# Kernel optimization log

Hardware: AMD Instinct MI355X
Metric: run time of the kernel (lower is better)

The kernel has to match this reference:

```python
import jax, jax.numpy as jnp
import numpy as np

N_SRC, N_DST, N_EDGES = 50000, 50000, 500000
IN_DIM, OUT_DIM, EDGE_DIM = 128, 128, 11
BN_EPS = 1e-5


def setup_inputs() -> dict:
    key = jax.random.key(0)
    ks = jax.random.split(key, 16)
    s = 0.05
    return {
        "src_feat": jax.random.normal(ks[0], (N_SRC, IN_DIM), jnp.float32),
        "dst_feat": jax.random.normal(ks[1], (N_DST, IN_DIM), jnp.float32),
        "edge_feats": jax.random.normal(ks[2], (N_EDGES, EDGE_DIM), jnp.float32),
        "src_idx": jax.random.randint(ks[3], (N_EDGES,), 0, N_SRC, jnp.int32),
        "dst_idx": jax.random.randint(ks[4], (N_EDGES,), 0, N_DST, jnp.int32),
        "W_src": jax.random.normal(ks[5], (IN_DIM, OUT_DIM), jnp.float32) * s,
        "b_src": jnp.zeros((OUT_DIM,), jnp.float32),
        "W_dst": jax.random.normal(ks[6], (IN_DIM, OUT_DIM), jnp.float32) * s,
        "b_dst": jnp.zeros((OUT_DIM,), jnp.float32),
        "W_edge": jax.random.normal(ks[7], (EDGE_DIM, OUT_DIM), jnp.float32) * s,
        "b_edge": jnp.zeros((OUT_DIM,), jnp.float32),
        "attn_w": jax.random.normal(ks[8], (3 * OUT_DIM,), jnp.float32) * s,
        "attn_b": jnp.zeros((), jnp.float32),
        "gamma": jnp.ones((OUT_DIM,), jnp.float32),
        "beta": jnp.zeros((OUT_DIM,), jnp.float32),
        "alpha": jnp.asarray(0.25, jnp.float32),
    }


def reference(src_feat, dst_feat, edge_feats, src_idx, dst_idx,
              W_src, b_src, W_dst, b_dst, W_edge, b_edge,
              attn_w, attn_b, gamma, beta, alpha):
    D = W_src.shape[1]
    # project at node/edge level (math identical to projecting gathered feats)
    hs = src_feat @ W_src + b_src            # [Ns, D]  (linear_src)
    hd = dst_feat @ W_dst + b_dst            # [Nd, D]  (linear_dst)
    ep = edge_feats @ W_edge + b_edge        # [E, D]   (linear_edge)
    # attn_l on concat([src, dst, edge]) == sum of three dot products + bias
    aw_s, aw_d, aw_e = attn_w[:D], attn_w[D:2 * D], attn_w[2 * D:]
    a = (hs @ aw_s)[src_idx] + (hd @ aw_d)[dst_idx] + ep @ aw_e + attn_b  # [E]
    # edge softmax over incoming edges of each dst node
    n_dst = dst_feat.shape[0]
    seg_max = jax.ops.segment_max(a, dst_idx, num_segments=n_dst)
    a_exp = jnp.exp(a - seg_max[dst_idx])
    denom = jax.ops.segment_sum(a_exp, dst_idx, num_segments=n_dst)
    attn = a_exp / denom[dst_idx]            # [E]
    # weighted message = attn * linear_src(src_h); scatter-sum to dst
    msg = attn[:, None] * hs[src_idx]        # [E, D]
    h_new = jax.ops.segment_sum(msg, dst_idx, num_segments=n_dst)  # [Nd, D]
    # BatchNorm1d (training-mode batch statistics)
    mean = jnp.mean(h_new, axis=0)
    var = jnp.var(h_new, axis=0)
    h_bn = (h_new - mean) / jnp.sqrt(var + BN_EPS) * gamma + beta
    # PReLU (single shared alpha); dropout is identity in eval
    return jnp.where(h_bn >= 0, h_bn, alpha * h_bn)
```

## Files before the change

kernel.cpp:

```cpp
#include <hip/hip_runtime.h>
#include <cstddef>

#define NSRC 50000
#define NDST 50000
#define NEDGE 500000
#define DIM 128
#define EDIM 11
#define BN_EPS 1e-5f
#define SCAN_NBLK ((NDST + 255) / 256)

#define HS_BLOCKS ((NSRC + 63) / 64)
#define SCORE_BLK ((NDST + 63) / 64)
#define EDB       ((NEDGE + 511) / 512)
#define SC_BLOCKS ((NEDGE + 1023) / 1024)
#define FUSE_GRID (196 * 9)

typedef short bf16x8 __attribute__((ext_vector_type(8)));
typedef float f32x4 __attribute__((ext_vector_type(4)));

#define OFF_HS       0
#define OFF_SSCORE   (OFF_HS + (size_t)NSRC*DIM/2)
#define OFF_DSCORE   (OFF_SSCORE + NSRC)
#define OFF_DEG16    (OFF_DSCORE + NDST)
#define OFF_COLSUM   (OFF_DEG16 + (size_t)NDST*16)
#define OFF_COLSQ    (OFF_COLSUM + 128)
#define OFF_OFFS     (OFF_COLSQ + 128)
#define OFF_REW      (OFF_OFFS + NDST + 2)
#define OFF_PAIRS    (OFF_REW + 2*(size_t)NEDGE)
#define OFF_WDVEC    (OFF_PAIRS + 2*(size_t)NEDGE)
#define OFF_WEVEC    (OFF_WDVEC + 128)
#define OFF_SCAL     (OFF_WEVEC + 16)
#define OFF_WSVEC    (OFF_SCAL + 4)
#define OFF_PART     (OFF_WSVEC + 128)
#define OFF_WT       (((OFF_PART + 256 + 3) / 4) * 4)

__device__ __forceinline__ unsigned short f2bf(float x) {
    unsigned int u = __float_as_uint(x);
    u += 0x7FFFu + ((u >> 16) & 1u);
    return (unsigned short)(u >> 16);
}
__device__ __forceinline__ float bf2f(unsigned int u16) {
    return __uint_as_float(u16 << 16);
}

__global__ __launch_bounds__(256) void k_prepwt(const float* __restrict__ W_dst,
                                                const float* __restrict__ b_dst,
                                                const float* __restrict__ W_edge,
                                                const float* __restrict__ b_edge,
                                                const float* __restrict__ W_src,
                                                const float* __restrict__ b_src,
                                                const float* __restrict__ attn_w,
                                                const float* __restrict__ attn_b,
                                                float* __restrict__ wd_vec,
                                                float* __restrict__ we_vec,
                                                float* __restrict__ ws_vec,
                                                float* __restrict__ scal,
                                                unsigned short* __restrict__ wt) {
    int bb = blockIdx.x;
    int t = threadIdx.x;
    __shared__ float red[128];
    __shared__ float tile[32][33];
    if (bb == 0) {
        if (t < 128) {
            float acc = 0.f;
            for (int d = 0; d < DIM; ++d) acc += W_dst[t * DIM + d] * attn_w[DIM + d];
            wd_vec[t] = acc;
            red[t] = b_dst[t] * attn_w[DIM + t];
        }
        __syncthreads();
        for (int s = 64; s > 0; s >>= 1) { if (t < s) red[t] += red[t + s]; __syncthreads(); }
        if (t == 0) scal[0] = red[0];
    } else if (bb == 1) {
        if (t < 128) {
            if (t < EDIM) {
                float e = 0.f;
                for (int d = 0; d < DIM; ++d) e += W_edge[t * DIM + d] * attn_w[2 * DIM + d];
                we_vec[t] = e;
            }
            red[t] = b_edge[t] * attn_w[2 * DIM + t];
        }
        __syncthreads();
        for (int s = 64; s > 0; s >>= 1) { if (t < s) red[t] += red[t + s]; __syncthreads(); }
        if (t == 0) scal[1] = red[0] + attn_b[0];
    } else if (bb == 2) {
        if (t < 128) {
            float acc = 0.f;
            for (int d = 0; d < DIM; ++d) acc += W_src[t * DIM + d] * attn_w[d];
            ws_vec[t] = acc;
            red[t] = b_src[t] * attn_w[t];
        }
        __syncthreads();
        for (int s = 64; s > 0; s >>= 1) { if (t < s) red[t] += red[t + s]; __syncthreads(); }
        if (t == 0) scal[2] = red[0];
    } else {
        int idx = bb - 3;
        int bi = idx & 3;
        int bj = idx >> 2;
        int cl = t & 31;
        #pragma unroll
        for (int i = 0; i < 4; ++i) {
            int kl = (t >> 5) * 4 + i;
            tile[kl][cl] = W_src[(size_t)(bi * 32 + kl) * DIM + bj * 32 + cl];
        }
        __syncthreads();
        int ko = t & 31;
        #pragma unroll
        for (int i = 0; i < 4; ++i) {
            int co = (t >> 5) * 4 + i;
            wt[(size_t)(bj * 32 + co) * DIM + bi * 32 + ko] = f2bf(tile[ko][co]);
        }
    }
}

__global__ __launch_bounds__(256) void k_score(const float* __restrict__ src_feat,
                                               const float* __restrict__ dst_feat,
                                               const float* __restrict__ ws_vec,
                                               const float* __restrict__ wd_vec,
                                               const float* __restrict__ scal,
                                               float* __restrict__ s_score,
                                               float* __restrict__ d_score) {
    int bid = blockIdx.x;
    const float* X;
    const float* V;
    float* out;
    float c;
    int r0;
    if (bid < SCORE_BLK) {
        X = src_feat; V = ws_vec; out = s_score; c = scal[2]; r0 = bid * 64;
    } else {
        X = dst_feat; V = wd_vec; out = d_score; c = scal[0]; r0 = (bid - SCORE_BLK) * 64;
    }
    int t = threadIdx.x;
    int row = r0 + (t >> 2);
    int c0 = (t & 3) * 32;
    if (row >= NDST) return;
    const float4* x = reinterpret_cast<const float4*>(X + (size_t)row * DIM + c0);
    const float4* w = reinterpret_cast<const float4*>(V + c0);
    float p = 0.f;
    #pragma unroll
    for (int i = 0; i < 8; ++i) {
        float4 a = x[i], b = w[i];
        p += a.x * b.x + a.y * b.y + a.z * b.z + a.w * b.w;
    }
    p += __shfl_xor(p, 1);
    p += __shfl_xor(p, 2);
    if ((t & 3) == 0) out[row] = p + c;
}

__global__ __launch_bounds__(256, 2) void k_fused(const float* __restrict__ A,
                                               const unsigned short* __restrict__ wt,
                                               const float* __restrict__ bias,
                                               const float* __restrict__ ef,
                                               const int* __restrict__ src_idx,
                                               const int* __restrict__ dst_idx,
                                               const float* __restrict__ s_score,
                                               const float* __restrict__ d_score,
                                               const float* __restrict__ we_vec,
                                               const float* __restrict__ scal,
                                               unsigned short* __restrict__ hsb,
                                               int2* __restrict__ rew,
                                               int* __restrict__ deg16) {
    const int g = blockIdx.x / 9;
    const int sl = blockIdx.x % 9;
    const int t = threadIdx.x;

    if (sl < 4) {
        const int hb = g * 4 + sl;
        if (hb >= HS_BLOCKS) return;
        const int wv = t >> 6;
        const int lane = t & 63;
        const int lrow = lane & 15;
        const int kg = lane >> 4;
        const int grow = hb * 64 + wv * 16 + lrow;
        const bool rowok = grow < NSRC;
        const float* arow = A + (size_t)grow * DIM;

        bf16x8 af[4];
        #pragma unroll
        for (int s = 0; s < 4; ++s) {
            float4 p0 = make_float4(0.f, 0.f, 0.f, 0.f), p1 = p0;
            if (rowok) {
                p0 = *reinterpret_cast<const float4*>(arow + 32 * s + kg * 8);
                p1 = *reinterpret_cast<const float4*>(arow + 32 * s + kg * 8 + 4);
            }
            bf16x8 a;
            a[0] = (short)f2bf(p0.x); a[1] = (short)f2bf(p0.y);
            a[2] = (short)f2bf(p0.z); a[3] = (short)f2bf(p0.w);
            a[4] = (short)f2bf(p1.x); a[5] = (short)f2bf(p1.y);
            a[6] = (short)f2bf(p1.z); a[7] = (short)f2bf(p1.w);
            af[s] = a;
        }

        f32x4 acc[8];
        #pragma unroll
        for (int c = 0; c < 8; ++c) acc[c] = (f32x4){0.f, 0.f, 0.f, 0.f};

        #pragma unroll
        for (int c = 0; c < 8; ++c) {
            #pragma unroll
            for (int s = 0; s < 4; ++s) {
                const bf16x8 b = *reinterpret_cast<const bf16x8*>(
                    wt + ((size_t)(16 * c + lrow) * DIM + 32 * s + kg * 8));
                acc[c] = __builtin_amdgcn_mfma_f32_16x16x32_bf16(af[s], b, acc[c], 0, 0, 0);
            }
        }

        const int orow0 = hb * 64 + wv * 16 + kg * 4;
        #pragma unroll
        for (int c = 0; c < 8; ++c) {
            float bb = bias[16 * c + lrow];
            #pragma unroll
            for (int i = 0; i < 4; ++i) {
                unsigned int mybf = f2bf(acc[c][i] + bb);
                unsigned int nb = (unsigned int)__shfl_xor((int)mybf, 1);
                int orow = orow0 + i;
                if ((lrow & 1) == 0 && orow < NSRC) {
                    *reinterpret_cast<unsigned int*>(hsb + (size_t)orow * DIM + 16 * c + lrow)
                        = (mybf & 0xFFFFu) | (nb << 16);
                }
            }
        }
    } else {
        const int eb = g * 5 + (sl - 4);
        if (eb >= EDB) return;
        float wvv[EDIM];
        #pragma unroll
        for (int k = 0; k < EDIM; ++k) wvv[k] = we_vec[k];
        const float s1 = scal[1];
        int ebase = eb * 512 + t;
        #pragma unroll
        for (int i = 0; i < 2; ++i) {
            int e = ebase + i * 256;
            if (e < NEDGE) {
                int s = src_idx[e], d = dst_idx[e];
                const float* er = ef + (size_t)e * EDIM;
                float a = s1;
                #pragma unroll
                for (int k = 0; k < EDIM; ++k) a += er[k] * wvv[k];
                a += s_score[s] + d_score[d];
                float w = expf(a);
                int r = atomicAdd(&deg16[(size_t)d * 16], 1);
                rew[e] = make_int2(r, __float_as_int(w));
            }
        }
    }
}

__global__ __launch_bounds__(256) void k_scanA(const int* __restrict__ deg16,
                                               int* __restrict__ offL,
                                               int* __restrict__ partials) {
    __shared__ int tmp[256];
    int t = threadIdx.x;
    int i = blockIdx.x * 256 + t;
    int v = (i < NDST) ? deg16[(size_t)i * 16] : 0;
    tmp[t] = v;
    __syncthreads();
    #pragma unroll
    for (int d = 1; d < 256; d <<= 1) {
        int u = (t >= d) ? tmp[t - d] : 0;
        __syncthreads();
        tmp[t] += u;
        __syncthreads();
    }
    if (i < NDST) offL[i] = tmp[t] - v;
    if (t == 255) partials[blockIdx.x] = tmp[255];
}

__global__ __launch_bounds__(256) void k_scanB(int* __restrict__ partials) {
    __shared__ int tmp[256];
    int t = threadIdx.x;
    int v = (t < SCAN_NBLK) ? partials[t] : 0;
    tmp[t] = v;
    __syncthreads();
    #pragma unroll
    for (int d = 1; d < 256; d <<= 1) {
        int u = (t >= d) ? tmp[t - d] : 0;
        __syncthreads();
        tmp[t] += u;
        __syncthreads();
    }
    if (t < SCAN_NBLK) partials[t] = tmp[t] - v;
}

__global__ __launch_bounds__(256) void k_scat(const int* __restrict__ src_idx,
                                              const int* __restrict__ dst_idx,
                                              const int2* __restrict__ rew,
                                              const int* __restrict__ offL,
                                              const int* __restrict__ part,
                                              int2* __restrict__ pairs) {
    int base = blockIdx.x * 1024 + threadIdx.x;
    #pragma unroll
    for (int i = 0; i < 4; ++i) {
        int e = base + i * 256;
        if (e < NEDGE) {
            int d = dst_idx[e];
            int2 r = rew[e];
            int pos = offL[d] + part[d >> 8] + r.x;
            pairs[pos] = make_int2(src_idx[e], r.y);
        }
    }
}

__global__ __launch_bounds__(256) void k_gather(const unsigned short* __restrict__ hsb,
                                                const int* __restrict__ offL,
                                                const int* __restrict__ part,
                                                const int2* __restrict__ pairs,
                                                float* __restrict__ h_new) {
    int wid = (blockIdx.x * blockDim.x + threadIdx.x) >> 6;
    int lane = threadIdx.x & 63;
    if (wid >= NDST) return;
    int b = offL[wid] + part[wid >> 8];
    int e2 = (wid + 1 < NDST) ? (offL[wid + 1] + part[(wid + 1) >> 8]) : NEDGE;
    int deg = e2 - b;
    const int half = lane >> 5;
    const int c8 = lane & 31;
    float a0 = 0.f, a1 = 0.f, a2 = 0.f, a3 = 0.f, wsum = 0.f;

    for (int base = 0; base < deg; base += 64) {
        int cnt = min(deg - base, 64);
        int myS = 0;
        float myW = 0.f;
        if (lane < cnt) {
            int2 p = pairs[b + base + lane];
            myS = p.x;
            myW = __int_as_float(p.y);
        }
        wsum += myW;

        int j = 0;
        for (; j + 8 <= cnt; j += 8) {
            #pragma unroll
            for (int q = 0; q < 4; ++q) {
                int jj = j + 2 * q + half;
                int s0 = __shfl(myS, jj);
                float w0 = __shfl(myW, jj);
                uint2 v = *reinterpret_cast<const uint2*>(hsb + (size_t)s0 * DIM + c8 * 4);
                a0 += w0 * bf2f(v.x & 0xFFFFu);
                a1 += w0 * bf2f(v.x >> 16);
                a2 += w0 * bf2f(v.y & 0xFFFFu);
                a3 += w0 * bf2f(v.y >> 16);
            }
        }
        for (; j < cnt; j += 2) {
            int jj = j + half;
            int s0 = __shfl(myS, jj);
            float w0 = __shfl(myW, jj);
            uint2 v = *reinterpret_cast<const uint2*>(hsb + (size_t)s0 * DIM + c8 * 4);
            a0 += w0 * bf2f(v.x & 0xFFFFu);
            a1 += w0 * bf2f(v.x >> 16);
            a2 += w0 * bf2f(v.y & 0xFFFFu);
            a3 += w0 * bf2f(v.y >> 16);
        }
    }

    a0 += __shfl_xor(a0, 32);
    a1 += __shfl_xor(a1, 32);
    a2 += __shfl_xor(a2, 32);
    a3 += __shfl_xor(a3, 32);
    #pragma unroll
    for (int m = 1; m < 64; m <<= 1) wsum += __shfl_xor(wsum, m);

    float inv = (deg > 0) ? 1.f / wsum : 0.f;
    if (half == 0) {
        reinterpret_cast<float4*>(h_new + (size_t)wid * DIM)[c8]
            = make_float4(a0 * inv, a1 * inv, a2 * inv, a3 * inv);
    }
}

__global__ __launch_bounds__(256) void k_bnstats(const float* __restrict__ h,
                                                 float* __restrict__ colsum,
                                                 float* __restrict__ colsq) {
    int col = threadIdx.x & 127;
    int rp = threadIdx.x >> 7;
    float s = 0.f, q = 0.f;
    for (int r = blockIdx.x * 2 + rp; r < NDST; r += gridDim.x * 2) {
        float x = h[(size_t)r * DIM + col];
        s += x;
        q += x * x;
    }
    __shared__ float ls[2][128], lq[2][128];
    ls[rp][col] = s;
    lq[rp][col] = q;
    __syncthreads();
    if (rp == 0) {
        atomicAdd(&colsum[col], ls[0][col] + ls[1][col]);
        atomicAdd(&colsq[col], lq[0][col] + lq[1][col]);
    }
}

__global__ __launch_bounds__(256) void k_bnfinal(float* __restrict__ h,
                                                 const float* __restrict__ colsum,
                                                 const float* __restrict__ colsq,
                                                 const float* __restrict__ gamma,
                                                 const float* __restrict__ beta,
                                                 const float* __restrict__ alpha_p) {
    const size_t total4 = (size_t)NDST * DIM / 4;
    const float alpha = alpha_p[0];
    const float invN = 1.f / (float)NDST;
    const int c0 = (threadIdx.x & 31) * 4;
    float sc[4], sh[4];
    #pragma unroll
    for (int k = 0; k < 4; ++k) {
        float mean = colsum[c0 + k] * invN;
        float var = colsq[c0 + k] * invN - mean * mean;
        float s = gamma[c0 + k] * rsqrtf(var + BN_EPS);
        sc[k] = s;
        sh[k] = beta[c0 + k] - mean * s;
    }
    size_t stride = (size_t)gridDim.x * blockDim.x;
    for (size_t i = blockIdx.x * blockDim.x + threadIdx.x; i < total4; i += stride) {
        float4 x = reinterpret_cast<float4*>(h)[i];
        float y0 = x.x * sc[0] + sh[0];
        float y1 = x.y * sc[1] + sh[1];
        float y2 = x.z * sc[2] + sh[2];
        float y3 = x.w * sc[3] + sh[3];
        float4 o;
        o.x = y0 >= 0.f ? y0 : alpha * y0;
        o.y = y1 >= 0.f ? y1 : alpha * y1;
        o.z = y2 >= 0.f ? y2 : alpha * y2;
        o.w = y3 >= 0.f ? y3 : alpha * y3;
        reinterpret_cast<float4*>(h)[i] = o;
    }
}

extern "C" void kernel_launch(void* const* d_in, const int* in_sizes, int n_in,
                              void* d_out, int out_size, void* d_ws, size_t ws_size,
                              hipStream_t stream) {
    const float* src_feat   = (const float*)d_in[0];
    const float* dst_feat   = (const float*)d_in[1];
    const float* edge_feats = (const float*)d_in[2];
    const int*   src_idx    = (const int*)d_in[3];
    const int*   dst_idx    = (const int*)d_in[4];
    const float* W_src      = (const float*)d_in[5];
    const float* b_src      = (const float*)d_in[6];
    const float* W_dst      = (const float*)d_in[7];
    const float* b_dst      = (const float*)d_in[8];
    const float* W_edge     = (const float*)d_in[9];
    const float* b_edge     = (const float*)d_in[10];
    const float* attn_w     = (const float*)d_in[11];
    const float* attn_b     = (const float*)d_in[12];
    const float* gamma      = (const float*)d_in[13];
    const float* beta       = (const float*)d_in[14];
    const float* alpha      = (const float*)d_in[15];

    float* ws      = (float*)d_ws;
    unsigned short* hsb = (unsigned short*)(ws + OFF_HS);
    float* s_score = ws + OFF_SSCORE;
    float* d_score = ws + OFF_DSCORE;
    int*   deg16   = (int*)(ws + OFF_DEG16);
    float* colsum  = ws + OFF_COLSUM;
    float* colsq   = ws + OFF_COLSQ;
    int*   offL    = (int*)(ws + OFF_OFFS);
    int2*  rew     = (int2*)(ws + OFF_REW);
    int2*  pairs   = (int2*)(ws + OFF_PAIRS);
    float* wd_vec  = ws + OFF_WDVEC;
    float* we_vec  = ws + OFF_WEVEC;
    float* scal    = ws + OFF_SCAL;
    float* ws_vec  = ws + OFF_WSVEC;
    int*   part    = (int*)(ws + OFF_PART);
    unsigned short* wt = (unsigned short*)(ws + OFF_WT);

    float* h_new = (float*)d_out;

    hipMemsetAsync(deg16, 0, ((size_t)NDST * 16 + 256) * sizeof(int), stream);

    k_prepwt<<<19, 256, 0, stream>>>(W_dst, b_dst, W_edge, b_edge, W_src, b_src,
                                     attn_w, attn_b, wd_vec, we_vec, ws_vec, scal, wt);
    k_score<<<2 * SCORE_BLK, 256, 0, stream>>>(src_feat, dst_feat, ws_vec, wd_vec,
                                               scal, s_score, d_score);
    k_fused<<<FUSE_GRID, 256, 0, stream>>>(src_feat, wt, b_src, edge_feats,
                                           src_idx, dst_idx, s_score, d_score,
                                           we_vec, scal, hsb, rew, deg16);
    k_scanA<<<SCAN_NBLK, 256, 0, stream>>>(deg16, offL, part);
    k_scanB<<<1, 256, 0, stream>>>(part);
    k_scat<<<SC_BLOCKS, 256, 0, stream>>>(src_idx, dst_idx, rew, offL, part, pairs);
    k_gather<<<(NDST * 64 + 255) / 256, 256, 0, stream>>>(hsb, offL, part, pairs, h_new);
    k_bnstats<<<512, 256, 0, stream>>>(h_new, colsum, colsq);
    k_bnfinal<<<1024, 256, 0, stream>>>(h_new, colsum, colsq, gamma, beta, alpha);
}
```

Before: 143.5 us.

## Fold node score kernel into fused projection kernel and defer exp to scatter

Removes the separate k_score launch by giving the fused kernel four extra block slots per group that compute the source and destination attention scores. The edge branch now stores only the edge-feature logit and the rank. The score gather and exp move into k_scat, which runs after the scores are complete. This saves a launch and lets score work overlap with the GEMM and edge work, at the cost of extra random score loads in the scatter kernel.

```diff
diff --git a/kernel.cpp b/kernel.cpp
--- a/kernel.cpp
+++ b/kernel.cpp
@@ -10,10 +10,10 @@
 #define SCAN_NBLK ((NDST + 255) / 256)
 
 #define HS_BLOCKS ((NSRC + 63) / 64)
-#define SCORE_BLK ((NDST + 63) / 64)
+#define SCB       ((NSRC + 127) / 128)
 #define EDB       ((NEDGE + 511) / 512)
 #define SC_BLOCKS ((NEDGE + 1023) / 1024)
-#define FUSE_GRID (196 * 9)
+#define FUSE_GRID (196 * 13)
 
 typedef short bf16x8 __attribute__((ext_vector_type(8)));
 typedef float f32x4 __attribute__((ext_vector_type(4)));
@@ -25,8 +25,8 @@
 #define OFF_COLSUM   (OFF_DEG16 + (size_t)NDST*16)
 #define OFF_COLSQ    (OFF_COLSUM + 128)
 #define OFF_OFFS     (OFF_COLSQ + 128)
-#define OFF_REW      (OFF_OFFS + NDST + 2)
-#define OFF_PAIRS    (OFF_REW + 2*(size_t)NEDGE)
+#define OFF_EER      (OFF_OFFS + NDST + 2)
+#define OFF_PAIRS    (OFF_EER + 2*(size_t)NEDGE)
 #define OFF_WDVEC    (OFF_PAIRS + 2*(size_t)NEDGE)
 #define OFF_WEVEC    (OFF_WDVEC + 128)
 #define OFF_SCAL     (OFF_WEVEC + 16)
@@ -112,56 +112,23 @@
     }
 }
 
-__global__ __launch_bounds__(256) void k_score(const float* __restrict__ src_feat,
-                                               const float* __restrict__ dst_feat,
-                                               const float* __restrict__ ws_vec,
-                                               const float* __restrict__ wd_vec,
-                                               const float* __restrict__ scal,
-                                               float* __restrict__ s_score,
-                                               float* __restrict__ d_score) {
-    int bid = blockIdx.x;
-    const float* X;
-    const float* V;
-    float* out;
-    float c;
-    int r0;
-    if (bid < SCORE_BLK) {
-        X = src_feat; V = ws_vec; out = s_score; c = scal[2]; r0 = bid * 64;
-    } else {
-        X = dst_feat; V = wd_vec; out = d_score; c = scal[0]; r0 = (bid - SCORE_BLK) * 64;
-    }
-    int t = threadIdx.x;
-    int row = r0 + (t >> 2);
-    int c0 = (t & 3) * 32;
-    if (row >= NDST) return;
-    const float4* x = reinterpret_cast<const float4*>(X + (size_t)row * DIM + c0);
-    const float4* w = reinterpret_cast<const float4*>(V + c0);
-    float p = 0.f;
-    #pragma unroll
-    for (int i = 0; i < 8; ++i) {
-        float4 a = x[i], b = w[i];
-        p += a.x * b.x + a.y * b.y + a.z * b.z + a.w * b.w;
-    }
-    p += __shfl_xor(p, 1);
-    p += __shfl_xor(p, 2);
-    if ((t & 3) == 0) out[row] = p + c;
-}
-
 __global__ __launch_bounds__(256, 2) void k_fused(const float* __restrict__ A,
                                                const unsigned short* __restrict__ wt,
                                                const float* __restrict__ bias,
                                                const float* __restrict__ ef,
-                                               const int* __restrict__ src_idx,
+                                               const float* __restrict__ dst_feat,
                                                const int* __restrict__ dst_idx,
-                                               const float* __restrict__ s_score,
-                                               const float* __restrict__ d_score,
+                                               const float* __restrict__ ws_vec,
+                                               const float* __restrict__ wd_vec,
                                                const float* __restrict__ we_vec,
                                                const float* __restrict__ scal,
                                                unsigned short* __restrict__ hsb,
-                                               int2* __restrict__ rew,
+                                               float* __restrict__ s_score,
+                                               float* __restrict__ d_score,
+                                               int2* __restrict__ eer,
                                                int* __restrict__ deg16) {
-    const int g = blockIdx.x / 9;
-    const int sl = blockIdx.x % 9;
+    const int g = blockIdx.x / 13;
+    const int sl = blockIdx.x % 13;
     const int t = threadIdx.x;
 
     if (sl < 4) {
@@ -220,8 +187,34 @@
                 }
             }
         }
+    } else if (sl < 8) {
+        int idx = g * 4 + (sl - 4);
+        const float* X;
+        const float* V;
+        float* out;
+        float c;
+        if (idx < SCB) {
+            X = A; V = ws_vec; out = s_score; c = scal[2];
+        } else {
+            idx -= SCB;
+            if (idx >= SCB) return;
+            X = dst_feat; V = wd_vec; out = d_score; c = scal[0];
+        }
+        int row = idx * 128 + (t >> 1);
+        int c0 = (t & 1) * 64;
+        if (row >= NDST) return;
+        const float4* x = reinterpret_cast<const float4*>(X + (size_t)row * DIM + c0);
+        const float4* w = reinterpret_cast<const float4*>(V + c0);
+        float p = 0.f;
+        #pragma unroll
+        for (int i = 0; i < 16; ++i) {
+            float4 a = x[i], b = w[i];
+            p += a.x * b.x + a.y * b.y + a.z * b.z + a.w * b.w;
+        }
+        p += __shfl_xor(p, 1);
+        if ((t & 1) == 0) out[row] = p + c;
     } else {
-        const int eb = g * 5 + (sl - 4);
+        const int eb = g * 5 + (sl - 8);
         if (eb >= EDB) return;
         float wvv[EDIM];
         #pragma unroll
@@ -232,15 +225,13 @@
         for (int i = 0; i < 2; ++i) {
             int e = ebase + i * 256;
             if (e < NEDGE) {
-                int s = src_idx[e], d = dst_idx[e];
+                int d = dst_idx[e];
                 const float* er = ef + (size_t)e * EDIM;
                 float a = s1;
                 #pragma unroll
                 for (int k = 0; k < EDIM; ++k) a += er[k] * wvv[k];
-                a += s_score[s] + d_score[d];
-                float w = expf(a);
                 int r = atomicAdd(&deg16[(size_t)d * 16], 1);
-                rew[e] = make_int2(r, __float_as_int(w));
+                eer[e] = make_int2(r, __float_as_int(a));
             }
         }
     }
@@ -284,7 +275,9 @@
 
 __global__ __launch_bounds__(256) void k_scat(const int* __restrict__ src_idx,
                                               const int* __restrict__ dst_idx,
-                                              const int2* __restrict__ rew,
+                                              const int2* __restrict__ eer,
+                                              const float* __restrict__ s_score,
+                                              const float* __restrict__ d_score,
                                               const int* __restrict__ offL,
                                               const int* __restrict__ part,
                                               int2* __restrict__ pairs) {
@@ -293,10 +286,11 @@
     for (int i = 0; i < 4; ++i) {
         int e = base + i * 256;
         if (e < NEDGE) {
-            int d = dst_idx[e];
-            int2 r = rew[e];
-            int pos = offL[d] + part[d >> 8] + r.x;
-            pairs[pos] = make_int2(src_idx[e], r.y);
+            int s = src_idx[e], d = dst_idx[e];
+            int2 re = eer[e];
+            float w = expf(__int_as_float(re.y) + s_score[s] + d_score[d]);
+            int pos = offL[d] + part[d >> 8] + re.x;
+            pairs[pos] = make_int2(s, __float_as_int(w));
         }
     }
 }
@@ -451,7 +445,7 @@
     float* colsum  = ws + OFF_COLSUM;
     float* colsq   = ws + OFF_COLSQ;
     int*   offL    = (int*)(ws + OFF_OFFS);
-    int2*  rew     = (int2*)(ws + OFF_REW);
+    int2*  eer     = (int2*)(ws + OFF_EER);
     int2*  pairs   = (int2*)(ws + OFF_PAIRS);
     float* wd_vec  = ws + OFF_WDVEC;
     float* we_vec  = ws + OFF_WEVEC;
@@ -466,14 +460,14 @@
 
     k_prepwt<<<19, 256, 0, stream>>>(W_dst, b_dst, W_edge, b_edge, W_src, b_src,
                                      attn_w, attn_b, wd_vec, we_vec, ws_vec, scal, wt);
-    k_score<<<2 * SCORE_BLK, 256, 0, stream>>>(src_feat, dst_feat, ws_vec, wd_vec,
-                                               scal, s_score, d_score);
     k_fused<<<FUSE_GRID, 256, 0, stream>>>(src_feat, wt, b_src, edge_feats,
-                                           src_idx, dst_idx, s_score, d_score,
-                                           we_vec, scal, hsb, rew, deg16);
+                                           dst_feat, dst_idx, ws_vec, wd_vec,
+                                           we_vec, scal, hsb, s_score, d_score,
+                                           eer, deg16);
     k_scanA<<<SCAN_NBLK, 256, 0, stream>>>(deg16, offL, part);
     k_scanB<<<1, 256, 0, stream>>>(part);
-    k_scat<<<SC_BLOCKS, 256, 0, stream>>>(src_idx, dst_idx, rew, offL, part, pairs);
+    k_scat<<<SC_BLOCKS, 256, 0, stream>>>(src_idx, dst_idx, eer, s_score, d_score,
+                                          offL, part, pairs);
     k_gather<<<(NDST * 64 + 255) / 256, 256, 0, stream>>>(hsb, offL, part, pairs, h_new);
     k_bnstats<<<512, 256, 0, stream>>>(h_new, colsum, colsq);
     k_bnfinal<<<1024, 256, 0, stream>>>(h_new, colsum, colsq, gamma, beta, alpha);
```

New measurement: 134.9 us, median of 2. 6.0% less time.
